# Kernel optimization log

Hardware: AMD Instinct MI355X
Metric: run time of the kernel (lower is better)

The kernel has to match this reference:

```python
import jax, jax.numpy as jnp
import numpy as np

EMBED = 1024
HEADS = 16
HEAD_DIM = EMBED // HEADS
MLP_HIDDEN = 4096


def _layernorm(x, g, b, eps=1e-5):
    mu = jnp.mean(x, axis=-1, keepdims=True)
    var = jnp.mean(jnp.square(x - mu), axis=-1, keepdims=True)
    return (x - mu) * jax.lax.rsqrt(var + eps) * g + b


def setup_inputs() -> dict:
    key = jax.random.key(0)
    ks = jax.random.split(key, 8)
    s = 0.02
    return {
        "x": jax.random.normal(ks[0], (8, 1024, EMBED), dtype=jnp.float32),
        "qkv_w": jax.random.normal(ks[1], (EMBED, 3 * EMBED), dtype=jnp.float32) * s,
        "qkv_b": jnp.zeros((3 * EMBED,), jnp.float32),
        "proj_w": jax.random.normal(ks[2], (EMBED, EMBED), dtype=jnp.float32) * s,
        "proj_b": jnp.zeros((EMBED,), jnp.float32),
        "fc1_w": jax.random.normal(ks[3], (EMBED, MLP_HIDDEN), dtype=jnp.float32) * s,
        "fc1_b": jnp.zeros((MLP_HIDDEN,), jnp.float32),
        "fc2_w": jax.random.normal(ks[4], (MLP_HIDDEN, EMBED), dtype=jnp.float32) * s,
        "fc2_b": jnp.zeros((EMBED,), jnp.float32),
        "ln1_g": jnp.ones((EMBED,), jnp.float32),
        "ln1_b": jnp.zeros((EMBED,), jnp.float32),
        "ln2_g": jnp.ones((EMBED,), jnp.float32),
        "ln2_b": jnp.zeros((EMBED,), jnp.float32),
    }


def reference(x, qkv_w, qkv_b, proj_w, proj_b, fc1_w, fc1_b, fc2_w, fc2_b,
              ln1_g, ln1_b, ln2_g, ln2_b):
    B, N, C = x.shape
    scale = HEAD_DIM ** -0.5

    # --- MHSA on pre-norm input ---
    h = _layernorm(x, ln1_g, ln1_b)
    qkv = h @ qkv_w + qkv_b                      # [B,N,3C]
    qkv = qkv.reshape(B, N, 3, HEADS, HEAD_DIM)
    q, k, v = (qkv[:, :, i].transpose(0, 2, 1, 3) for i in range(3))  # [B,H,N,d]
    attn = jnp.einsum('bhqd,bhkd->bhqk', q, k) * scale
    attn = jax.nn.softmax(attn, axis=-1)
    o = jnp.einsum('bhqk,bhkd->bhqd', attn, v)   # [B,H,N,d]
    o = o.transpose(0, 2, 1, 3).reshape(B, N, C)
    x = x + (o @ proj_w + proj_b)

    # --- MLP ---
    h2 = _layernorm(x, ln2_g, ln2_b)
    h2 = jax.nn.gelu(h2 @ fc1_w + fc1_b, approximate=False)
    x = x + (h2 @ fc2_w + fc2_b)
    return x
```

## Files before the change

### kernel.cpp

```cpp
#include <hip/hip_runtime.h>
#include <hip/hip_bf16.h>

typedef __bf16 bf16x8 __attribute__((ext_vector_type(8)));
typedef float  f32x4  __attribute__((ext_vector_type(4)));
typedef unsigned short u16;

static __device__ __forceinline__ u16 f2bf(float f) {
  union { float f; unsigned u; } v; v.f = f;
  unsigned r = v.u + 0x7fffu + ((v.u >> 16) & 1u);
  return (u16)(r >> 16);
}

static __device__ __forceinline__ void gld16(const void* g, void* l) {
  __builtin_amdgcn_global_load_lds(
      (const __attribute__((address_space(1))) unsigned int*)g,
      (__attribute__((address_space(3))) unsigned int*)l, 16, 0, 0);
}

#define SBAR() do { __builtin_amdgcn_sched_barrier(0); \
                    __builtin_amdgcn_s_barrier(); \
                    __builtin_amdgcn_sched_barrier(0); } while (0)

__global__ __launch_bounds__(256) void transpose_cast_k(
    const float* __restrict__ W, u16* __restrict__ Wt, int K, int N) {
  __shared__ float tile[32][33];
  const int t = threadIdx.x;
  const int n0 = blockIdx.x * 32, k0 = blockIdx.y * 32;
  const int r = t >> 3, c4 = (t & 7) * 4;
  const float4 v = *(const float4*)(W + (size_t)(k0 + r) * N + n0 + c4);
  tile[r][c4 + 0] = v.x; tile[r][c4 + 1] = v.y;
  tile[r][c4 + 2] = v.z; tile[r][c4 + 3] = v.w;
  __syncthreads();
  const int n = t >> 3, k4 = (t & 7) * 4;
  uint2 pk;
  pk.x = f2bf(tile[k4 + 0][n]) | ((unsigned)f2bf(tile[k4 + 1][n]) << 16);
  pk.y = f2bf(tile[k4 + 2][n]) | ((unsigned)f2bf(tile[k4 + 3][n]) << 16);
  *(uint2*)(Wt + (size_t)(n0 + n) * K + k0 + k4) = pk;
}

__global__ __launch_bounds__(256) void ln_cast_k(
    const float* __restrict__ x, const float* __restrict__ g,
    const float* __restrict__ b, u16* __restrict__ out) {
  __shared__ float red[2][4];
  const int t = threadIdx.x;
  const size_t row = blockIdx.x;
  const float4 v = *(const float4*)(x + row * 1024 + t * 4);
  float s = v.x + v.y + v.z + v.w;
  float ss = v.x * v.x + v.y * v.y + v.z * v.z + v.w * v.w;
  #pragma unroll
  for (int m = 1; m <= 32; m <<= 1) { s += __shfl_xor(s, m); ss += __shfl_xor(ss, m); }
  if ((t & 63) == 0) { red[0][t >> 6] = s; red[1][t >> 6] = ss; }
  __syncthreads();
  s  = red[0][0] + red[0][1] + red[0][2] + red[0][3];
  ss = red[1][0] + red[1][1] + red[1][2] + red[1][3];
  const float mu = s * (1.f / 1024.f);
  const float var = ss * (1.f / 1024.f) - mu * mu;
  const float rs = rsqrtf(var + 1e-5f);
  const float4 gv = *(const float4*)(g + t * 4);
  const float4 bv = *(const float4*)(b + t * 4);
  uint2 pk;
  pk.x = f2bf((v.x - mu) * rs * gv.x + bv.x) |
         ((unsigned)f2bf((v.y - mu) * rs * gv.y + bv.y) << 16);
  pk.y = f2bf((v.z - mu) * rs * gv.z + bv.z) |
         ((unsigned)f2bf((v.w - mu) * rs * gv.w + bv.w) << 16);
  *(uint2*)(out + row * 1024 + t * 4) = pk;
}

template <int EPI, int WN>
__global__ __launch_bounds__(512, 2) void gemm8_k(
    const u16* __restrict__ A, const u16* __restrict__ Bt,
    const float* __restrict__ bias, u16* __restrict__ Cb, float* __restrict__ Cf,
    const float* __restrict__ R, u16* __restrict__ vT, int M, int N, int K) {
  constexpr int MR = 2 * WN;
  constexpr int BN = 64 * WN;
  constexpr int SHSZ = 32768 + WN * 8192;
  __shared__ u16 SH[SHSZ];
  const int t = threadIdx.x;
  const int nt = N / BN;
  const int q = gridDim.x >> 3;
  const int swz = (blockIdx.x & 7) * q + (blockIdx.x >> 3);
  const int tn = swz % nt, tm = swz / nt;
  const int lo = t & 15, hi = (t >> 4) & 3, wid = t >> 6;
  const int wm = wid / WN, wn = wid & (WN - 1);
  const int NT = K >> 6;

  const int srow = t >> 3;
  const int sc = (t & 7) ^ (srow & 7);
  const u16* gA = A  + (size_t)(tm * 256) * K;
  const u16* gB = Bt + (size_t)(tn * BN) * K;
  auto stA = [&](int dd, int c, int T) {
    gld16(gA + (size_t)(c * 64 + srow) * K + (size_t)T * 64 + sc * 8,
          &SH[dd * 16384 + c * 4096 + t * 8]);
  };
  auto stB = [&](int dd, int c, int T) {
    gld16(gB + (size_t)(c * 64 + srow) * K + (size_t)T * 64 + sc * 8,
          &SH[32768 + dd * (WN * 4096) + c * 4096 + t * 8]);
  };

  const int xr = lo & 7;
  const int rowA = wm * (MR * 16) + lo;
  const int rowB = wn * 64 + lo;
#define RD_A(d, m, kk) (*(const bf16x8*)&SH[(d)*16384 + (rowA + (m)*16)*64 + ((((kk)<<2)+hi)^xr)*8])
#define RD_B(d, n, kk) (*(const bf16x8*)&SH[32768 + (d)*(WN*4096) + (rowB + (n)*16)*64 + ((((kk)<<2)+hi)^xr)*8])
#define MF(a, b, c) __builtin_amdgcn_mfma_f32_16x16x32_bf16(a, b, c, 0, 0, 0)

  f32x4 acc[MR][4];
  #pragma unroll
  for (int i = 0; i < MR; ++i)
    #pragma unroll
    for (int j = 0; j < 4; ++j) acc[i][j] = (f32x4){0.f, 0.f, 0.f, 0.f};

#define PH16(d, M0, M1, STAGES, WAITS) do { \
    bf16x8 a0 = RD_A(d, M0, 0), a1 = RD_A(d, M0, 1); \
    bf16x8 a2 = RD_A(d, M1, 0), a3 = RD_A(d, M1, 1); \
    STAGES; SBAR(); __builtin_amdgcn_s_setprio(1); \
    acc[M0][0]=MF(a0,b00,acc[M0][0]); acc[M0][1]=MF(a0,b10,acc[M0][1]); \
    acc[M0][2]=MF(a0,b20,acc[M0][2]); acc[M0][3]=MF(a0,b30,acc[M0][3]); \
    acc[M1][0]=MF(a2,b00,acc[M1][0]); acc[M1][1]=MF(a2,b10,acc[M1][1]); \
    acc[M1][2]=MF(a2,b20,acc[M1][2]); acc[M1][3]=MF(a2,b30,acc[M1][3]); \
    acc[M0][0]=MF(a1,b01,acc[M0][0]); acc[M0][1]=MF(a1,b11,acc[M0][1]); \
    acc[M0][2]=MF(a1,b21,acc[M0][2]); acc[M0][3]=MF(a1,b31,acc[M0][3]); \
    acc[M1][0]=MF(a3,b01,acc[M1][0]); acc[M1][1]=MF(a3,b11,acc[M1][1]); \
    acc[M1][2]=MF(a3,b21,acc[M1][2]); acc[M1][3]=MF(a3,b31,acc[M1][3]); \
    __builtin_amdgcn_s_setprio(0); WAITS; SBAR(); } while (0)

#define PH8(d, M0, STAGES, WAITS) do { \
    bf16x8 a0 = RD_A(d, M0, 0), a1 = RD_A(d, M0, 1); \
    STAGES; SBAR(); __builtin_amdgcn_s_setprio(1); \
    acc[M0][0]=MF(a0,b00,acc[M0][0]); acc[M0][1]=MF(a0,b10,acc[M0][1]); \
    acc[M0][2]=MF(a0,b20,acc[M0][2]); acc[M0][3]=MF(a0,b30,acc[M0][3]); \
    acc[M0][0]=MF(a1,b01,acc[M0][0]); acc[M0][1]=MF(a1,b11,acc[M0][1]); \
    acc[M0][2]=MF(a1,b21,acc[M0][2]); acc[M0][3]=MF(a1,b31,acc[M0][3]); \
    __builtin_amdgcn_s_setprio(0); WAITS; SBAR(); } while (0)

  if constexpr (WN == 4) {
    stA(0, 0, 0); stA(0, 1, 0); stA(0, 2, 0); stA(0, 3, 0);
    stB(0, 0, 0); stB(0, 1, 0); stB(0, 2, 0); stB(0, 3, 0);
    stB(1, 0, 1); stB(1, 1, 1); stB(1, 2, 1); stB(1, 3, 1);
    stA(1, 0, 1); stA(1, 2, 1);
    asm volatile("s_waitcnt vmcnt(6)" ::: "memory");
    SBAR();
    for (int T = 0; T < NT; ++T) {
      const int d = T & 1, dn = d ^ 1;
      bf16x8 b00 = RD_B(d,0,0), b01 = RD_B(d,0,1), b10 = RD_B(d,1,0), b11 = RD_B(d,1,1);
      bf16x8 b20 = RD_B(d,2,0), b21 = RD_B(d,2,1), b30 = RD_B(d,3,0), b31 = RD_B(d,3,1);
      PH16(d, 0, 1, { if (T + 1 < NT) { stA(dn, 1, T + 1); stA(dn, 3, T + 1); } }, );
      PH16(d, 2, 3, { if (T + 2 < NT) { stB(d, 0, T + 2); stB(d, 1, T + 2); } }, );
      PH16(d, 4, 5, { if (T + 2 < NT) { stB(d, 2, T + 2); stB(d, 3, T + 2); } }, );
      PH16(d, 6, 7, { if (T + 2 < NT) { stA(d, 0, T + 2); stA(d, 2, T + 2); } },
           { if (T < NT - 2)       { asm volatile("s_waitcnt vmcnt(6)" ::: "memory"); }
             else if (T == NT - 2) { asm volatile("s_waitcnt vmcnt(0)" ::: "memory"); } });
    }
  } else {
    stA(0, 0, 0); stA(0, 1, 0); stA(0, 2, 0); stA(0, 3, 0);
    stB(0, 0, 0); stB(0, 1, 0);
    stB(1, 0, 1); stB(1, 1, 1);
    asm volatile("s_waitcnt vmcnt(2)" ::: "memory");
    SBAR();
    for (int T = 0; T < NT; ++T) {
      const int d = T & 1, dn = d ^ 1;
      bf16x8 b00 = RD_B(d,0,0), b01 = RD_B(d,0,1), b10 = RD_B(d,1,0), b11 = RD_B(d,1,1);
      bf16x8 b20 = RD_B(d,2,0), b21 = RD_B(d,2,1), b30 = RD_B(d,3,0), b31 = RD_B(d,3,1);
      PH8(d, 0, { if (T + 1 < NT) { stA(dn, 0, T + 1); stA(dn, 1, T + 1);
                                    stA(dn, 2, T + 1); stA(dn, 3, T + 1); } }, );
      PH8(d, 1, { if (T + 2 < NT) { stB(d, 0, T + 2); stB(d, 1, T + 2); } }, );
      PH8(d, 2, , );
      PH8(d, 3, ,
          { if (T < NT - 2)       { asm volatile("s_waitcnt vmcnt(2)" ::: "memory"); }
            else if (T == NT - 2) { asm volatile("s_waitcnt vmcnt(0)" ::: "memory"); } });
    }
  }

  if constexpr (EPI == 2) {
    #pragma unroll
    for (int ni = 0; ni < 4; ++ni) {
      const int col = tn * BN + wn * 64 + ni * 16 + lo;
      const float bv = bias[col];
      #pragma unroll
      for (int mi = 0; mi < MR; ++mi) {
        const int row0 = tm * 256 + wm * (MR * 16) + mi * 16 + hi * 4;
        #pragma unroll
        for (int r = 0; r < 4; ++r) {
          const size_t idx = (size_t)(row0 + r) * N + col;
          Cf[idx] = acc[mi][ni][r] + bv + R[idx];
        }
      }
    }
  } else {
    #pragma unroll
    for (int ni = 0; ni < 4; ++ni) {
      const int colL = wn * 64 + ni * 16 + lo;
      const float bv = bias[tn * BN + colL];
      #pragma unroll
      for (int mi = 0; mi < MR; ++mi) {
        const int rowL = wm * (MR * 16) + mi * 16 + hi * 4;
        #pragma unroll
        for (int r = 0; r < 4; ++r) {
          float val = acc[mi][ni][r] + bv;
          if (EPI == 1) {
            const float u = 0.79788456f * val * (1.f + 0.044715f * val * val);
            const float e = __expf(fminf(2.f * u, 80.f));
            val = val * (e / (e + 1.f));
          }
          SH[(rowL + r) * BN + colL] = f2bf(val);
        }
      }
    }
    __syncthreads();
    constexpr int ROWSH = (BN == 256) ? 9 : 8;
    const int base = t * 16;
    #pragma unroll
    for (int p = 0; p < BN / 16; ++p) {
      const int o = base + p * 8192;
      const int row = o >> ROWSH;
      const int cb = (o & (2 * BN - 1)) >> 1;
      const uint4 v4 = *(const uint4*)&SH[o >> 1];
      *(uint4*)(Cb + (size_t)(tm * 256 + row) * N + tn * BN + cb) = v4;
    }
    if constexpr (EPI == 3) {
      if (tn >= 8) {
        const int c = t & 255;
        const int rg = t >> 8;
        const int gcol = tn * 256 + c;
        const int hh = (gcol - 2048) >> 6, dd = gcol & 63;
        const int bb = tm >> 2, nb = (tm & 3) * 256;
        u16* dst = vT + ((size_t)((bb * 16 + hh) * 64 + dd) << 10) + nb + rg * 128;
        #pragma unroll
        for (int i = 0; i < 16; ++i) {
          const int r0 = rg * 128 + i * 8;
          u16 tv[8];
          #pragma unroll
          for (int j = 0; j < 8; ++j) tv[j] = SH[(r0 + j) * 256 + c];
          uint4 pk;
          pk.x = tv[0] | ((unsigned)tv[1] << 16);
          pk.y = tv[2] | ((unsigned)tv[3] << 16);
          pk.z = tv[4] | ((unsigned)tv[5] << 16);
          pk.w = tv[6] | ((unsigned)tv[7] << 16);
          *(uint4*)(dst + i * 8) = pk;
        }
      }
    }
  }
#undef RD_A
#undef RD_B
#undef MF
#undef PH16
#undef PH8
}

__global__ __launch_bounds__(256, 2) void attn_k(
    const u16* __restrict__ qkv, const u16* __restrict__ vT, u16* __restrict__ o) {
  __shared__ u16 lK[64 * 64];
  __shared__ u16 lV[64 * 64];
  __shared__ u16 lP[64 * 72];
  const int t = threadIdx.x;
  const int lo = t & 15, hi = (t >> 4) & 3, w = t >> 6;
  const int swz = (blockIdx.x & 7) * 256 + (blockIdx.x >> 3);
  const int qt = swz & 15, bh = swz >> 4;
  const int b = bh >> 4, h = bh & 15;
  const int q0 = qt * 64;
  const u16* Qb = qkv + (size_t)b * 1024 * 3072 + h * 64;
  const u16* Kb = Qb + 1024;
  const u16* Vt = vT + (size_t)bh * 64 * 1024;

  bf16x8 qf[2];
  {
    const size_t q = q0 + w * 16 + lo;
    qf[0] = *(const bf16x8*)(Qb + q * 3072 + hi * 8);
    qf[1] = *(const bf16x8*)(Qb + q * 3072 + 32 + hi * 8);
  }
  f32x4 oacc[4];
  #pragma unroll
  for (int i = 0; i < 4; ++i) oacc[i] = (f32x4){0.f, 0.f, 0.f, 0.f};
  float m = -1e30f, lsum = 0.f;
  const int srow = t >> 3;
  const int sc = (t & 7) ^ (srow & 7);
  const int xr = lo & 7;
  const float SC = 0.125f * 1.44269504f;

  for (int kv0 = 0; kv0 < 1024; kv0 += 64) {
    __syncthreads();
    #pragma unroll
    for (int j = 0; j < 2; ++j) {
      const int r64 = j * 32 + srow;
      gld16(Kb + (size_t)(kv0 + r64) * 3072 + sc * 8, &lK[(j * 256 + t) * 8]);
      gld16(Vt + (size_t)r64 * 1024 + kv0 + sc * 8, &lV[(j * 256 + t) * 8]);
    }
    __syncthreads();

    f32x4 s[4];
    #pragma unroll
    for (int i = 0; i < 4; ++i) s[i] = (f32x4){0.f, 0.f, 0.f, 0.f};
    #pragma unroll
    for (int kk = 0; kk < 2; ++kk) {
      #pragma unroll
      for (int mi = 0; mi < 4; ++mi) {
        const bf16x8 kf = *(const bf16x8*)&lK[(mi * 16 + lo) * 64 + (((kk << 2) + hi) ^ xr) * 8];
        s[mi] = __builtin_amdgcn_mfma_f32_16x16x32_bf16(kf, qf[kk], s[mi], 0, 0, 0);
      }
    }
    float sv[16];
    float tmax = -1e30f;
    #pragma unroll
    for (int mi = 0; mi < 4; ++mi)
      #pragma unroll
      for (int r = 0; r < 4; ++r) {
        const float xx = s[mi][r] * SC;
        sv[mi * 4 + r] = xx;
        tmax = fmaxf(tmax, xx);
      }
    tmax = fmaxf(tmax, __shfl_xor(tmax, 16));
    tmax = fmaxf(tmax, __shfl_xor(tmax, 32));
    if (__any(tmax > m + 11.5f)) {
      const float mnew = fmaxf(m, tmax);
      const float alpha = exp2f(m - mnew);
      m = mnew;
      lsum *= alpha;
      float ar[4];
      #pragma unroll
      for (int r = 0; r < 4; ++r) ar[r] = __shfl(alpha, hi * 4 + r);
      #pragma unroll
      for (int ni = 0; ni < 4; ++ni)
        #pragma unroll
        for (int r = 0; r < 4; ++r) oacc[ni][r] *= ar[r];
    }
    float p[16], ts = 0.f;
    #pragma unroll
    for (int i = 0; i < 16; ++i) { p[i] = exp2f(sv[i] - m); ts += p[i]; }
    ts += __shfl_xor(ts, 16);
    ts += __shfl_xor(ts, 32);
    lsum += ts;
    #pragma unroll
    for (int mi = 0; mi < 4; ++mi) {
      uint2 pk;
      pk.x = f2bf(p[mi * 4 + 0]) | ((unsigned)f2bf(p[mi * 4 + 1]) << 16);
      pk.y = f2bf(p[mi * 4 + 2]) | ((unsigned)f2bf(p[mi * 4 + 3]) << 16);
      *(uint2*)&lP[(w * 16 + lo) * 72 + mi * 16 + hi * 4] = pk;
    }
    asm volatile("s_waitcnt lgkmcnt(0)" ::: "memory");
    #pragma unroll
    for (int kk = 0; kk < 2; ++kk) {
      const bf16x8 pf = *(const bf16x8*)&lP[(w * 16 + lo) * 72 + kk * 32 + hi * 8];
      #pragma unroll
      for (int ni = 0; ni < 4; ++ni) {
        const bf16x8 vf = *(const bf16x8*)&lV[(ni * 16 + lo) * 64 + (((kk << 2) + hi) ^ xr) * 8];
        oacc[ni] = __builtin_amdgcn_mfma_f32_16x16x32_bf16(pf, vf, oacc[ni], 0, 0, 0);
      }
    }
  }
  float lr[4];
  #pragma unroll
  for (int r = 0; r < 4; ++r) lr[r] = 1.f / __shfl(lsum, hi * 4 + r);
  #pragma unroll
  for (int ni = 0; ni < 4; ++ni) {
    const int d = ni * 16 + lo;
    #pragma unroll
    for (int r = 0; r < 4; ++r) {
      const int n = q0 + w * 16 + hi * 4 + r;
      o[((size_t)(b * 1024 + n) * 16 + h) * 64 + d] = f2bf(oacc[ni][r] * lr[r]);
    }
  }
}

extern "C" void kernel_launch(void* const* d_in, const int* in_sizes, int n_in,
                              void* d_out, int out_size, void* d_ws, size_t ws_size,
                              hipStream_t stream) {
  const float* x      = (const float*)d_in[0];
  const float* qkv_w  = (const float*)d_in[1];
  const float* qkv_b  = (const float*)d_in[2];
  const float* proj_w = (const float*)d_in[3];
  const float* proj_b = (const float*)d_in[4];
  const float* fc1_w  = (const float*)d_in[5];
  const float* fc1_b  = (const float*)d_in[6];
  const float* fc2_w  = (const float*)d_in[7];
  const float* fc2_b  = (const float*)d_in[8];
  const float* ln1_g  = (const float*)d_in[9];
  const float* ln1_b  = (const float*)d_in[10];
  const float* ln2_g  = (const float*)d_in[11];
  const float* ln2_b  = (const float*)d_in[12];
  float* out = (float*)d_out;
  char* ws = (char*)d_ws;
  u16* wqkvT = (u16*)(ws);
  u16* wprojT = (u16*)(ws + 6291456);
  u16* wfc1T = (u16*)(ws + 8388608);
  u16* wfc2T = (u16*)(ws + 16777216);
  u16* hbuf  = (u16*)(ws + 25165824);
  u16* qkvo  = (u16*)(ws + 41943040);
  u16* vT    = (u16*)(ws + 92274688);
  u16* fc1o  = qkvo;

  transpose_cast_k<<<dim3(96, 32),  256, 0, stream>>>(qkv_w,  wqkvT, 1024, 3072);
  transpose_cast_k<<<dim3(32, 32),  256, 0, stream>>>(proj_w, wprojT, 1024, 1024);
  transpose_cast_k<<<dim3(128, 32), 256, 0, stream>>>(fc1_w,  wfc1T, 1024, 4096);
  transpose_cast_k<<<dim3(32, 128), 256, 0, stream>>>(fc2_w,  wfc2T, 4096, 1024);
  ln_cast_k<<<8192, 256, 0, stream>>>(x, ln1_g, ln1_b, hbuf);
  gemm8_k<3, 4><<<384, 512, 0, stream>>>(hbuf, wqkvT, qkv_b, qkvo, nullptr, nullptr, vT, 8192, 3072, 1024);
  attn_k<<<2048, 256, 0, stream>>>(qkvo, vT, hbuf);
  gemm8_k<2, 2><<<256, 512, 0, stream>>>(hbuf, wprojT, proj_b, nullptr, out, x, nullptr, 8192, 1024, 1024);
  ln_cast_k<<<8192, 256, 0, stream>>>(out, ln2_g, ln2_b, hbuf);
  gemm8_k<1, 4><<<512, 512, 0, stream>>>(hbuf, wfc1T, fc1_b, fc1o, nullptr, nullptr, nullptr, 8192, 4096, 1024);
  gemm8_k<2, 2><<<256, 512, 0, stream>>>(fc1o, wfc2T, fc2_b, nullptr, out, out, nullptr, 8192, 1024, 4096);
}
```

Before: 384.0 us.

## Use 16-wave 256x256 GEMM for QKV/FC1 and fuse prep kernels

Replaces the 8-wave 256x256 GEMM used for the QKV and FC1 projections with a 1024-thread, 16-wave kernel in which each wave owns a 64x64 sub-tile. The K-loop is reorganised into two MFMA phases per 64-wide K step, each preceded by loads for the next tile. The templated GEMM is split so the residual-add projections get their own 128-wide kernel. The four weight transpose-casts and the first LayerNorm are merged into a single launch to cut launch overhead. The larger block limits occupancy to one block per CU and changes register pressure.

```diff
diff --git a/kernel.cpp b/kernel.cpp
--- a/kernel.cpp
+++ b/kernel.cpp
@@ -21,21 +21,57 @@
                     __builtin_amdgcn_s_barrier(); \
                     __builtin_amdgcn_sched_barrier(0); } while (0)
 
-__global__ __launch_bounds__(256) void transpose_cast_k(
-    const float* __restrict__ W, u16* __restrict__ Wt, int K, int N) {
-  __shared__ float tile[32][33];
+__global__ __launch_bounds__(256) void prep_k(
+    const float* __restrict__ qkv_w, const float* __restrict__ proj_w,
+    const float* __restrict__ fc1_w, const float* __restrict__ fc2_w,
+    u16* __restrict__ wqkvT, u16* __restrict__ wprojT,
+    u16* __restrict__ wfc1T, u16* __restrict__ wfc2T,
+    const float* __restrict__ x, const float* __restrict__ g,
+    const float* __restrict__ b, u16* __restrict__ hbuf) {
+  const int bid = blockIdx.x;
   const int t = threadIdx.x;
-  const int n0 = blockIdx.x * 32, k0 = blockIdx.y * 32;
-  const int r = t >> 3, c4 = (t & 7) * 4;
-  const float4 v = *(const float4*)(W + (size_t)(k0 + r) * N + n0 + c4);
-  tile[r][c4 + 0] = v.x; tile[r][c4 + 1] = v.y;
-  tile[r][c4 + 2] = v.z; tile[r][c4 + 3] = v.w;
-  __syncthreads();
-  const int n = t >> 3, k4 = (t & 7) * 4;
-  uint2 pk;
-  pk.x = f2bf(tile[k4 + 0][n]) | ((unsigned)f2bf(tile[k4 + 1][n]) << 16);
-  pk.y = f2bf(tile[k4 + 2][n]) | ((unsigned)f2bf(tile[k4 + 3][n]) << 16);
-  *(uint2*)(Wt + (size_t)(n0 + n) * K + k0 + k4) = pk;
+  if (bid < 12288) {
+    __shared__ float tile[32][33];
+    const float* W; u16* Wt; int K, N, nx, i;
+    if (bid < 3072)      { W = qkv_w;  Wt = wqkvT;  K = 1024; N = 3072; nx = 96;  i = bid; }
+    else if (bid < 4096) { W = proj_w; Wt = wprojT; K = 1024; N = 1024; nx = 32;  i = bid - 3072; }
+    else if (bid < 8192) { W = fc1_w;  Wt = wfc1T;  K = 1024; N = 4096; nx = 128; i = bid - 4096; }
+    else                 { W = fc2_w;  Wt = wfc2T;  K = 4096; N = 1024; nx = 32;  i = bid - 8192; }
+    const int n0 = (i % nx) * 32, k0 = (i / nx) * 32;
+    const int r = t >> 3, c4 = (t & 7) * 4;
+    const float4 v = *(const float4*)(W + (size_t)(k0 + r) * N + n0 + c4);
+    tile[r][c4 + 0] = v.x; tile[r][c4 + 1] = v.y;
+    tile[r][c4 + 2] = v.z; tile[r][c4 + 3] = v.w;
+    __syncthreads();
+    const int n = t >> 3, k4 = (t & 7) * 4;
+    uint2 pk;
+    pk.x = f2bf(tile[k4 + 0][n]) | ((unsigned)f2bf(tile[k4 + 1][n]) << 16);
+    pk.y = f2bf(tile[k4 + 2][n]) | ((unsigned)f2bf(tile[k4 + 3][n]) << 16);
+    *(uint2*)(Wt + (size_t)(n0 + n) * K + k0 + k4) = pk;
+  } else {
+    __shared__ float red[2][4];
+    const size_t row = bid - 12288;
+    const float4 v = *(const float4*)(x + row * 1024 + t * 4);
+    float s = v.x + v.y + v.z + v.w;
+    float ss = v.x * v.x + v.y * v.y + v.z * v.z + v.w * v.w;
+    #pragma unroll
+    for (int m = 1; m <= 32; m <<= 1) { s += __shfl_xor(s, m); ss += __shfl_xor(ss, m); }
+    if ((t & 63) == 0) { red[0][t >> 6] = s; red[1][t >> 6] = ss; }
+    __syncthreads();
+    s  = red[0][0] + red[0][1] + red[0][2] + red[0][3];
+    ss = red[1][0] + red[1][1] + red[1][2] + red[1][3];
+    const float mu = s * (1.f / 1024.f);
+    const float var = ss * (1.f / 1024.f) - mu * mu;
+    const float rs = rsqrtf(var + 1e-5f);
+    const float4 gv = *(const float4*)(g + t * 4);
+    const float4 bv = *(const float4*)(b + t * 4);
+    uint2 pk;
+    pk.x = f2bf((v.x - mu) * rs * gv.x + bv.x) |
+           ((unsigned)f2bf((v.y - mu) * rs * gv.y + bv.y) << 16);
+    pk.y = f2bf((v.z - mu) * rs * gv.z + bv.z) |
+           ((unsigned)f2bf((v.w - mu) * rs * gv.w + bv.w) << 16);
+    *(uint2*)(hbuf + row * 1024 + t * 4) = pk;
+  }
 }
 
 __global__ __launch_bounds__(256) void ln_cast_k(
@@ -66,63 +102,190 @@
   *(uint2*)(out + row * 1024 + t * 4) = pk;
 }
 
-template <int EPI, int WN>
-__global__ __launch_bounds__(512, 2) void gemm8_k(
+template <int EPI>
+__global__ __launch_bounds__(1024, 1) void gemm16_k(
     const u16* __restrict__ A, const u16* __restrict__ Bt,
-    const float* __restrict__ bias, u16* __restrict__ Cb, float* __restrict__ Cf,
-    const float* __restrict__ R, u16* __restrict__ vT, int M, int N, int K) {
-  constexpr int MR = 2 * WN;
-  constexpr int BN = 64 * WN;
-  constexpr int SHSZ = 32768 + WN * 8192;
-  __shared__ u16 SH[SHSZ];
+    const float* __restrict__ bias, u16* __restrict__ Cb,
+    u16* __restrict__ vT, int M, int N, int K) {
+  __shared__ u16 SH[65536];
   const int t = threadIdx.x;
-  const int nt = N / BN;
+  const int nt = N >> 8;
   const int q = gridDim.x >> 3;
   const int swz = (blockIdx.x & 7) * q + (blockIdx.x >> 3);
   const int tn = swz % nt, tm = swz / nt;
   const int lo = t & 15, hi = (t >> 4) & 3, wid = t >> 6;
-  const int wm = wid / WN, wn = wid & (WN - 1);
+  const int wm = wid >> 2, wn = wid & 3;
   const int NT = K >> 6;
 
   const int srow = t >> 3;
   const int sc = (t & 7) ^ (srow & 7);
   const u16* gA = A  + (size_t)(tm * 256) * K;
-  const u16* gB = Bt + (size_t)(tn * BN) * K;
+  const u16* gB = Bt + (size_t)(tn * 256) * K;
+  auto stA = [&](int dd, int c, int T) {
+    gld16(gA + (size_t)(c * 128 + srow) * K + (size_t)T * 64 + sc * 8,
+          &SH[dd * 16384 + c * 8192 + t * 8]);
+  };
+  auto stB = [&](int dd, int c, int T) {
+    gld16(gB + (size_t)(c * 128 + srow) * K + (size_t)T * 64 + sc * 8,
+          &SH[32768 + dd * 16384 + c * 8192 + t * 8]);
+  };
+
+  const int xr = lo & 7;
+  const int rowA = wm * 64 + lo;
+  const int rowB = wn * 64 + lo;
+#define RD_A(d, m, kk) (*(const bf16x8*)&SH[(d)*16384 + (rowA + (m)*16)*64 + ((((kk)<<2)+hi)^xr)*8])
+#define RD_B(d, n, kk) (*(const bf16x8*)&SH[32768 + (d)*16384 + (rowB + (n)*16)*64 + ((((kk)<<2)+hi)^xr)*8])
+#define MF(a, b, c) __builtin_amdgcn_mfma_f32_16x16x32_bf16(a, b, c, 0, 0, 0)
+
+  f32x4 acc[4][4];
+  #pragma unroll
+  for (int i = 0; i < 4; ++i)
+    #pragma unroll
+    for (int j = 0; j < 4; ++j) acc[i][j] = (f32x4){0.f, 0.f, 0.f, 0.f};
+
+  stA(0, 0, 0); stA(0, 1, 0); stB(0, 0, 0); stB(0, 1, 0);
+  stB(1, 0, 1); stB(1, 1, 1);
+  asm volatile("s_waitcnt vmcnt(2)" ::: "memory");
+  SBAR();
+
+  for (int T = 0; T < NT; ++T) {
+    const int d = T & 1, dn = d ^ 1;
+    bf16x8 b00 = RD_B(d,0,0), b01 = RD_B(d,0,1), b10 = RD_B(d,1,0), b11 = RD_B(d,1,1);
+    bf16x8 b20 = RD_B(d,2,0), b21 = RD_B(d,2,1), b30 = RD_B(d,3,0), b31 = RD_B(d,3,1);
+    {
+      bf16x8 a0 = RD_A(d,0,0), a1 = RD_A(d,1,0), a2 = RD_A(d,2,0), a3 = RD_A(d,3,0);
+      if (T + 1 < NT) { stA(dn, 0, T + 1); stA(dn, 1, T + 1); }
+      SBAR();
+      __builtin_amdgcn_s_setprio(1);
+      acc[0][0]=MF(a0,b00,acc[0][0]); acc[0][1]=MF(a0,b10,acc[0][1]);
+      acc[0][2]=MF(a0,b20,acc[0][2]); acc[0][3]=MF(a0,b30,acc[0][3]);
+      acc[1][0]=MF(a1,b00,acc[1][0]); acc[1][1]=MF(a1,b10,acc[1][1]);
+      acc[1][2]=MF(a1,b20,acc[1][2]); acc[1][3]=MF(a1,b30,acc[1][3]);
+      acc[2][0]=MF(a2,b00,acc[2][0]); acc[2][1]=MF(a2,b10,acc[2][1]);
+      acc[2][2]=MF(a2,b20,acc[2][2]); acc[2][3]=MF(a2,b30,acc[2][3]);
+      acc[3][0]=MF(a3,b00,acc[3][0]); acc[3][1]=MF(a3,b10,acc[3][1]);
+      acc[3][2]=MF(a3,b20,acc[3][2]); acc[3][3]=MF(a3,b30,acc[3][3]);
+      __builtin_amdgcn_s_setprio(0);
+      SBAR();
+    }
+    {
+      bf16x8 a0 = RD_A(d,0,1), a1 = RD_A(d,1,1), a2 = RD_A(d,2,1), a3 = RD_A(d,3,1);
+      if (T + 2 < NT) { stB(d, 0, T + 2); stB(d, 1, T + 2); }
+      SBAR();
+      __builtin_amdgcn_s_setprio(1);
+      acc[0][0]=MF(a0,b01,acc[0][0]); acc[0][1]=MF(a0,b11,acc[0][1]);
+      acc[0][2]=MF(a0,b21,acc[0][2]); acc[0][3]=MF(a0,b31,acc[0][3]);
+      acc[1][0]=MF(a1,b01,acc[1][0]); acc[1][1]=MF(a1,b11,acc[1][1]);
+      acc[1][2]=MF(a1,b21,acc[1][2]); acc[1][3]=MF(a1,b31,acc[1][3]);
+      acc[2][0]=MF(a2,b01,acc[2][0]); acc[2][1]=MF(a2,b11,acc[2][1]);
+      acc[2][2]=MF(a2,b21,acc[2][2]); acc[2][3]=MF(a2,b31,acc[2][3]);
+      acc[3][0]=MF(a3,b01,acc[3][0]); acc[3][1]=MF(a3,b11,acc[3][1]);
+      acc[3][2]=MF(a3,b21,acc[3][2]); acc[3][3]=MF(a3,b31,acc[3][3]);
+      __builtin_amdgcn_s_setprio(0);
+      if (T < NT - 2)       { asm volatile("s_waitcnt vmcnt(2)" ::: "memory"); }
+      else if (T == NT - 2) { asm volatile("s_waitcnt vmcnt(0)" ::: "memory"); }
+      SBAR();
+    }
+  }
+
+  #pragma unroll
+  for (int ni = 0; ni < 4; ++ni) {
+    const int colL = wn * 64 + ni * 16 + lo;
+    const float bv = bias[tn * 256 + colL];
+    #pragma unroll
+    for (int mi = 0; mi < 4; ++mi) {
+      const int rowL = wm * 64 + mi * 16 + hi * 4;
+      #pragma unroll
+      for (int r = 0; r < 4; ++r) {
+        float val = acc[mi][ni][r] + bv;
+        if (EPI == 1) {
+          const float u = 0.79788456f * val * (1.f + 0.044715f * val * val);
+          const float e = __expf(fminf(2.f * u, 80.f));
+          val = val * (e / (e + 1.f));
+        }
+        SH[(rowL + r) * 256 + colL] = f2bf(val);
+      }
+    }
+  }
+  __syncthreads();
+  {
+    const int base = t * 16;
+    #pragma unroll
+    for (int p = 0; p < 8; ++p) {
+      const int o = base + p * 16384;
+      const int row = o >> 9;
+      const int cb = (o & 511) >> 1;
+      const uint4 v4 = *(const uint4*)&SH[o >> 1];
+      *(uint4*)(Cb + (size_t)(tm * 256 + row) * N + tn * 256 + cb) = v4;
+    }
+  }
+  if constexpr (EPI == 3) {
+    if (tn >= 8) {
+      const int c = t & 255;
+      const int rg = t >> 8;
+      const int gcol = tn * 256 + c;
+      const int hh = (gcol - 2048) >> 6, dd = gcol & 63;
+      const int bb = tm >> 2, nb = (tm & 3) * 256;
+      u16* dst = vT + ((size_t)((bb * 16 + hh) * 64 + dd) << 10) + nb + rg * 64;
+      #pragma unroll
+      for (int i = 0; i < 8; ++i) {
+        const int r0 = rg * 64 + i * 8;
+        u16 tv[8];
+        #pragma unroll
+        for (int j = 0; j < 8; ++j) tv[j] = SH[(r0 + j) * 256 + c];
+        uint4 pk;
+        pk.x = tv[0] | ((unsigned)tv[1] << 16);
+        pk.y = tv[2] | ((unsigned)tv[3] << 16);
+        pk.z = tv[4] | ((unsigned)tv[5] << 16);
+        pk.w = tv[6] | ((unsigned)tv[7] << 16);
+        *(uint4*)(dst + i * 8) = pk;
+      }
+    }
+  }
+#undef RD_A
+#undef RD_B
+#undef MF
+}
+
+__global__ __launch_bounds__(512, 2) void gemmP_k(
+    const u16* __restrict__ A, const u16* __restrict__ Bt,
+    const float* __restrict__ bias, float* __restrict__ Cf,
+    const float* __restrict__ R, int M, int N, int K) {
+  __shared__ u16 SH[49152];
+  const int t = threadIdx.x;
+  const int nt = N >> 7;
+  const int q = gridDim.x >> 3;
+  const int swz = (blockIdx.x & 7) * q + (blockIdx.x >> 3);
+  const int tn = swz % nt, tm = swz / nt;
+  const int lo = t & 15, hi = (t >> 4) & 3, wid = t >> 6;
+  const int wm = wid >> 1, wn = wid & 1;
+  const int NT = K >> 6;
+
+  const int srow = t >> 3;
+  const int sc = (t & 7) ^ (srow & 7);
+  const u16* gA = A  + (size_t)(tm * 256) * K;
+  const u16* gB = Bt + (size_t)(tn * 128) * K;
   auto stA = [&](int dd, int c, int T) {
     gld16(gA + (size_t)(c * 64 + srow) * K + (size_t)T * 64 + sc * 8,
           &SH[dd * 16384 + c * 4096 + t * 8]);
   };
   auto stB = [&](int dd, int c, int T) {
     gld16(gB + (size_t)(c * 64 + srow) * K + (size_t)T * 64 + sc * 8,
-          &SH[32768 + dd * (WN * 4096) + c * 4096 + t * 8]);
+          &SH[32768 + dd * 8192 + c * 4096 + t * 8]);
   };
 
   const int xr = lo & 7;
-  const int rowA = wm * (MR * 16) + lo;
+  const int rowA = wm * 64 + lo;
   const int rowB = wn * 64 + lo;
 #define RD_A(d, m, kk) (*(const bf16x8*)&SH[(d)*16384 + (rowA + (m)*16)*64 + ((((kk)<<2)+hi)^xr)*8])
-#define RD_B(d, n, kk) (*(const bf16x8*)&SH[32768 + (d)*(WN*4096) + (rowB + (n)*16)*64 + ((((kk)<<2)+hi)^xr)*8])
+#define RD_B(d, n, kk) (*(const bf16x8*)&SH[32768 + (d)*8192 + (rowB + (n)*16)*64 + ((((kk)<<2)+hi)^xr)*8])
 #define MF(a, b, c) __builtin_amdgcn_mfma_f32_16x16x32_bf16(a, b, c, 0, 0, 0)
 
-  f32x4 acc[MR][4];
-  #pragma unroll
-  for (int i = 0; i < MR; ++i)
+  f32x4 acc[4][4];
+  #pragma unroll
+  for (int i = 0; i < 4; ++i)
     #pragma unroll
     for (int j = 0; j < 4; ++j) acc[i][j] = (f32x4){0.f, 0.f, 0.f, 0.f};
-
-#define PH16(d, M0, M1, STAGES, WAITS) do { \
-    bf16x8 a0 = RD_A(d, M0, 0), a1 = RD_A(d, M0, 1); \
-    bf16x8 a2 = RD_A(d, M1, 0), a3 = RD_A(d, M1, 1); \
-    STAGES; SBAR(); __builtin_amdgcn_s_setprio(1); \
-    acc[M0][0]=MF(a0,b00,acc[M0][0]); acc[M0][1]=MF(a0,b10,acc[M0][1]); \
-    acc[M0][2]=MF(a0,b20,acc[M0][2]); acc[M0][3]=MF(a0,b30,acc[M0][3]); \
-    acc[M1][0]=MF(a2,b00,acc[M1][0]); acc[M1][1]=MF(a2,b10,acc[M1][1]); \
-    acc[M1][2]=MF(a2,b20,acc[M1][2]); acc[M1][3]=MF(a2,b30,acc[M1][3]); \
-    acc[M0][0]=MF(a1,b01,acc[M0][0]); acc[M0][1]=MF(a1,b11,acc[M0][1]); \
-    acc[M0][2]=MF(a1,b21,acc[M0][2]); acc[M0][3]=MF(a1,b31,acc[M0][3]); \
-    acc[M1][0]=MF(a3,b01,acc[M1][0]); acc[M1][1]=MF(a3,b11,acc[M1][1]); \
-    acc[M1][2]=MF(a3,b21,acc[M1][2]); acc[M1][3]=MF(a3,b31,acc[M1][3]); \
-    __builtin_amdgcn_s_setprio(0); WAITS; SBAR(); } while (0)
 
 #define PH8(d, M0, STAGES, WAITS) do { \
     bf16x8 a0 = RD_A(d, M0, 0), a1 = RD_A(d, M0, 1); \
@@ -133,118 +296,41 @@
     acc[M0][2]=MF(a1,b21,acc[M0][2]); acc[M0][3]=MF(a1,b31,acc[M0][3]); \
     __builtin_amdgcn_s_setprio(0); WAITS; SBAR(); } while (0)
 
-  if constexpr (WN == 4) {
-    stA(0, 0, 0); stA(0, 1, 0); stA(0, 2, 0); stA(0, 3, 0);
-    stB(0, 0, 0); stB(0, 1, 0); stB(0, 2, 0); stB(0, 3, 0);
-    stB(1, 0, 1); stB(1, 1, 1); stB(1, 2, 1); stB(1, 3, 1);
-    stA(1, 0, 1); stA(1, 2, 1);
-    asm volatile("s_waitcnt vmcnt(6)" ::: "memory");
-    SBAR();
-    for (int T = 0; T < NT; ++T) {
-      const int d = T & 1, dn = d ^ 1;
-      bf16x8 b00 = RD_B(d,0,0), b01 = RD_B(d,0,1), b10 = RD_B(d,1,0), b11 = RD_B(d,1,1);
-      bf16x8 b20 = RD_B(d,2,0), b21 = RD_B(d,2,1), b30 = RD_B(d,3,0), b31 = RD_B(d,3,1);
-      PH16(d, 0, 1, { if (T + 1 < NT) { stA(dn, 1, T + 1); stA(dn, 3, T + 1); } }, );
-      PH16(d, 2, 3, { if (T + 2 < NT) { stB(d, 0, T + 2); stB(d, 1, T + 2); } }, );
-      PH16(d, 4, 5, { if (T + 2 < NT) { stB(d, 2, T + 2); stB(d, 3, T + 2); } }, );
-      PH16(d, 6, 7, { if (T + 2 < NT) { stA(d, 0, T + 2); stA(d, 2, T + 2); } },
-           { if (T < NT - 2)       { asm volatile("s_waitcnt vmcnt(6)" ::: "memory"); }
-             else if (T == NT - 2) { asm volatile("s_waitcnt vmcnt(0)" ::: "memory"); } });
-    }
-  } else {
-    stA(0, 0, 0); stA(0, 1, 0); stA(0, 2, 0); stA(0, 3, 0);
-    stB(0, 0, 0); stB(0, 1, 0);
-    stB(1, 0, 1); stB(1, 1, 1);
-    asm volatile("s_waitcnt vmcnt(2)" ::: "memory");
-    SBAR();
-    for (int T = 0; T < NT; ++T) {
-      const int d = T & 1, dn = d ^ 1;
-      bf16x8 b00 = RD_B(d,0,0), b01 = RD_B(d,0,1), b10 = RD_B(d,1,0), b11 = RD_B(d,1,1);
-      bf16x8 b20 = RD_B(d,2,0), b21 = RD_B(d,2,1), b30 = RD_B(d,3,0), b31 = RD_B(d,3,1);
-      PH8(d, 0, { if (T + 1 < NT) { stA(dn, 0, T + 1); stA(dn, 1, T + 1);
-                                    stA(dn, 2, T + 1); stA(dn, 3, T + 1); } }, );
-      PH8(d, 1, { if (T + 2 < NT) { stB(d, 0, T + 2); stB(d, 1, T + 2); } }, );
-      PH8(d, 2, , );
-      PH8(d, 3, ,
-          { if (T < NT - 2)       { asm volatile("s_waitcnt vmcnt(2)" ::: "memory"); }
-            else if (T == NT - 2) { asm volatile("s_waitcnt vmcnt(0)" ::: "memory"); } });
-    }
-  }
-
-  if constexpr (EPI == 2) {
-    #pragma unroll
-    for (int ni = 0; ni < 4; ++ni) {
-      const int col = tn * BN + wn * 64 + ni * 16 + lo;
-      const float bv = bias[col];
-      #pragma unroll
-      for (int mi = 0; mi < MR; ++mi) {
-        const int row0 = tm * 256 + wm * (MR * 16) + mi * 16 + hi * 4;
-        #pragma unroll
-        for (int r = 0; r < 4; ++r) {
-          const size_t idx = (size_t)(row0 + r) * N + col;
-          Cf[idx] = acc[mi][ni][r] + bv + R[idx];
-        }
-      }
-    }
-  } else {
-    #pragma unroll
-    for (int ni = 0; ni < 4; ++ni) {
-      const int colL = wn * 64 + ni * 16 + lo;
-      const float bv = bias[tn * BN + colL];
-      #pragma unroll
-      for (int mi = 0; mi < MR; ++mi) {
-        const int rowL = wm * (MR * 16) + mi * 16 + hi * 4;
-        #pragma unroll
-        for (int r = 0; r < 4; ++r) {
-          float val = acc[mi][ni][r] + bv;
-          if (EPI == 1) {
-            const float u = 0.79788456f * val * (1.f + 0.044715f * val * val);
-            const float e = __expf(fminf(2.f * u, 80.f));
-            val = val * (e / (e + 1.f));
-          }
-          SH[(rowL + r) * BN + colL] = f2bf(val);
-        }
-      }
-    }
-    __syncthreads();
-    constexpr int ROWSH = (BN == 256) ? 9 : 8;
-    const int base = t * 16;
-    #pragma unroll
-    for (int p = 0; p < BN / 16; ++p) {
-      const int o = base + p * 8192;
-      const int row = o >> ROWSH;
-      const int cb = (o & (2 * BN - 1)) >> 1;
-      const uint4 v4 = *(const uint4*)&SH[o >> 1];
-      *(uint4*)(Cb + (size_t)(tm * 256 + row) * N + tn * BN + cb) = v4;
-    }
-    if constexpr (EPI == 3) {
-      if (tn >= 8) {
-        const int c = t & 255;
-        const int rg = t >> 8;
-        const int gcol = tn * 256 + c;
-        const int hh = (gcol - 2048) >> 6, dd = gcol & 63;
-        const int bb = tm >> 2, nb = (tm & 3) * 256;
-        u16* dst = vT + ((size_t)((bb * 16 + hh) * 64 + dd) << 10) + nb + rg * 128;
-        #pragma unroll
-        for (int i = 0; i < 16; ++i) {
-          const int r0 = rg * 128 + i * 8;
-          u16 tv[8];
-          #pragma unroll
-          for (int j = 0; j < 8; ++j) tv[j] = SH[(r0 + j) * 256 + c];
-          uint4 pk;
-          pk.x = tv[0] | ((unsigned)tv[1] << 16);
-          pk.y = tv[2] | ((unsigned)tv[3] << 16);
-          pk.z = tv[4] | ((unsigned)tv[5] << 16);
-          pk.w = tv[6] | ((unsigned)tv[7] << 16);
-          *(uint4*)(dst + i * 8) = pk;
-        }
+  stA(0, 0, 0); stA(0, 1, 0); stA(0, 2, 0); stA(0, 3, 0);
+  stB(0, 0, 0); stB(0, 1, 0);
+  stB(1, 0, 1); stB(1, 1, 1);
+  asm volatile("s_waitcnt vmcnt(2)" ::: "memory");
+  SBAR();
+  for (int T = 0; T < NT; ++T) {
+    const int d = T & 1, dn = d ^ 1;
+    bf16x8 b00 = RD_B(d,0,0), b01 = RD_B(d,0,1), b10 = RD_B(d,1,0), b11 = RD_B(d,1,1);
+    bf16x8 b20 = RD_B(d,2,0), b21 = RD_B(d,2,1), b30 = RD_B(d,3,0), b31 = RD_B(d,3,1);
+    PH8(d, 0, { if (T + 1 < NT) { stA(dn, 0, T + 1); stA(dn, 1, T + 1);
+                                  stA(dn, 2, T + 1); stA(dn, 3, T + 1); } }, );
+    PH8(d, 1, { if (T + 2 < NT) { stB(d, 0, T + 2); stB(d, 1, T + 2); } }, );
+    PH8(d, 2, , );
+    PH8(d, 3, ,
+        { if (T < NT - 2)       { asm volatile("s_waitcnt vmcnt(2)" ::: "memory"); }
+          else if (T == NT - 2) { asm volatile("s_waitcnt vmcnt(0)" ::: "memory"); } });
+  }
+
+  #pragma unroll
+  for (int ni = 0; ni < 4; ++ni) {
+    const int col = tn * 128 + wn * 64 + ni * 16 + lo;
+    const float bv = bias[col];
+    #pragma unroll
+    for (int mi = 0; mi < 4; ++mi) {
+      const int row0 = tm * 256 + wm * 64 + mi * 16 + hi * 4;
+      #pragma unroll
+      for (int r = 0; r < 4; ++r) {
+        const size_t idx = (size_t)(row0 + r) * N + col;
+        Cf[idx] = acc[mi][ni][r] + bv + R[idx];
       }
     }
   }
 #undef RD_A
 #undef RD_B
 #undef MF
-#undef PH16
 #undef PH8
 }
 
@@ -389,15 +475,13 @@
   u16* vT    = (u16*)(ws + 92274688);
   u16* fc1o  = qkvo;
 
-  transpose_cast_k<<<dim3(96, 32),  256, 0, stream>>>(qkv_w,  wqkvT, 1024, 3072);
-  transpose_cast_k<<<dim3(32, 32),  256, 0, stream>>>(proj_w, wprojT, 1024, 1024);
-  transpose_cast_k<<<dim3(128, 32), 256, 0, stream>>>(fc1_w,  wfc1T, 1024, 4096);
-  transpose_cast_k<<<dim3(32, 128), 256, 0, stream>>>(fc2_w,  wfc2T, 4096, 1024);
-  ln_cast_k<<<8192, 256, 0, stream>>>(x, ln1_g, ln1_b, hbuf);
-  gemm8_k<3, 4><<<384, 512, 0, stream>>>(hbuf, wqkvT, qkv_b, qkvo, nullptr, nullptr, vT, 8192, 3072, 1024);
+  prep_k<<<20480, 256, 0, stream>>>(qkv_w, proj_w, fc1_w, fc2_w,
+                                    wqkvT, wprojT, wfc1T, wfc2T,
+                                    x, ln1_g, ln1_b, hbuf);
+  gemm16_k<3><<<384, 1024, 0, stream>>>(hbuf, wqkvT, qkv_b, qkvo, vT, 8192, 3072, 1024);
   attn_k<<<2048, 256, 0, stream>>>(qkvo, vT, hbuf);
-  gemm8_k<2, 2><<<256, 512, 0, stream>>>(hbuf, wprojT, proj_b, nullptr, out, x, nullptr, 8192, 1024, 1024);
+  gemmP_k<<<256, 512, 0, stream>>>(hbuf, wprojT, proj_b, out, x, 8192, 1024, 1024);
   ln_cast_k<<<8192, 256, 0, stream>>>(out, ln2_g, ln2_b, hbuf);
-  gemm8_k<1, 4><<<512, 512, 0, stream>>>(hbuf, wfc1T, fc1_b, fc1o, nullptr, nullptr, nullptr, 8192, 4096, 1024);
-  gemm8_k<2, 2><<<256, 512, 0, stream>>>(fc1o, wfc2T, fc2_b, nullptr, out, out, nullptr, 8192, 1024, 4096);
-}
+  gemm16_k<1><<<512, 1024, 0, stream>>>(hbuf, wfc1T, fc1_b, fc1o, nullptr, 8192, 4096, 1024);
+  gemmP_k<<<256, 512, 0, stream>>>(fc1o, wfc2T, fc2_b, out, out, 8192, 1024, 4096);
+}
```

Result: no change. 391.4 us (+1.9%).
